# Kernel optimization log

Hardware: AMD Instinct MI355X
Metric: run time of the kernel (lower is better)

The kernel has to match this reference:

```python
import jax, jax.numpy as jnp
import numpy as np

DIMS = 3; B = 256; N = 256; K = 16; HID = 64; INC = 64; F = 64; EPG = 8192; DEPTH = 3
EPS = 1e-15


def setup_inputs() -> dict:
    key = jax.random.key(0)
    ks = jax.random.split(key, 16)
    E = B * EPG
    g = jnp.repeat(jnp.arange(B), EPG)
    row = (g * N + jax.random.randint(ks[0], (E,), 0, N)).astype(jnp.int32)
    col = (g * N + jax.random.randint(ks[1], (E,), 0, N)).astype(jnp.int32)
    edge_index = jnp.stack([row, col])
    edge_attr = jax.random.uniform(ks[2], (E, DIMS), dtype=jnp.float32)
    x = jax.random.normal(ks[3], (B * N, INC), dtype=jnp.float32)
    x_to_pool = jax.random.normal(ks[4], (B * N, F * DIMS), dtype=jnp.float32)
    batch = jnp.repeat(jnp.arange(B), N).astype(jnp.int32)
    def w(k, shape, fan):
        return (jax.random.normal(k, shape, dtype=jnp.float32) / np.float32(np.sqrt(fan)))
    return dict(
        x=x, edge_attr=edge_attr, x_to_pool=x_to_pool,
        Wm0=w(ks[5], (DIMS, INC, HID), INC), Ws0=w(ks[6], (DIMS, INC, HID), INC), b0=jnp.zeros((DIMS, HID), jnp.float32),
        Wm1=w(ks[7], (DIMS, HID, HID), HID), Ws1=w(ks[8], (DIMS, HID, HID), HID), b1=jnp.zeros((DIMS, HID), jnp.float32),
        Wm2=w(ks[9], (DIMS, HID, K), HID), Ws2=w(ks[10], (DIMS, HID, K), HID), b2=jnp.zeros((DIMS, K), jnp.float32),
        fcW1=w(ks[11], (HID * (DEPTH - 1) + K, 50), HID * (DEPTH - 1) + K), fcb1=jnp.zeros((50,), jnp.float32),
        fcW2=w(ks[12], (50, K), 50), fcb2=jnp.zeros((K,), jnp.float32),
        edge_index=edge_index, batch=batch,
    )


def reference(x, edge_attr, x_to_pool, Wm0, Ws0, b0, Wm1, Ws1, b1, Wm2, Ws2, b2,
              fcW1, fcb1, fcW2, fcb2, edge_index, batch):
    row, col = edge_index[0], edge_index[1]
    n_total = B * N

    # ---- batch_to_adj: scatter edge list into dense (dims, B, N, N) adjacency ----
    ge, rl, cl = row // N, row % N, col % N
    adj = jnp.zeros((DIMS, B, N, N), x.dtype).at[:, ge, rl, cl].add(edge_attr.T)

    # ---- ParallelResGraphConv: per-dim edge-weighted graph conv stack ----
    def gconv(h, we, Wm, Ws, b):
        agg = jax.ops.segment_sum(we[:, None] * h[col], row, num_segments=n_total)
        return jax.nn.relu(agg @ Wm + h @ Ws + b)

    assignments = []
    for d in range(DIMS):  # small fixed loop over parallel streams
        we = edge_attr[:, d]
        h0 = gconv(x, we, Wm0[d], Ws0[d], b0[d])
        h1 = gconv(h0, we, Wm1[d], Ws1[d], b1[d])
        h2 = gconv(h1, we, Wm2[d], Ws2[d], b2[d])
        conv_out = jnp.concatenate([h0, h1, h2], axis=-1)  # [BN, HID*2+K]
        logits = (conv_out @ fcW1 + fcb1) @ fcW2 + fcb2     # shared pool_fc
        assignments.append(logits)
    s = jax.nn.softmax(jnp.stack(assignments).reshape(DIMS, B, N, K), axis=-1)

    # ---- losses: modularity (edge gather) + entropy ----
    a_flat = s.reshape(DIMS, n_total, K)
    mod = jnp.float32(0.0)
    for d in range(DIMS):
        diff = a_flat[d, row] - a_flat[d, col]
        mod = mod + jnp.mean(edge_attr[:, d] * jnp.sum(diff * diff, axis=-1))
    ent = jnp.mean(jnp.sum(-s * jnp.log(s + EPS), axis=-1))
    loss = mod + ent

    # ---- DiffPool-style pooling ----
    xr = x_to_pool.reshape(n_total, F, DIMS)
    xr = jnp.transpose(xr, (2, 0, 1)).reshape(DIMS, B, N, F)
    px = jnp.einsum('dbnk,dbnf->dbkf', s, xr)
    tmp = jnp.einsum('dbnk,dbnm->dbkm', s, adj)
    padj = jnp.einsum('dbkm,dbml->dbkl', tmp, s)
    scale = jnp.float32(K / N)
    px = jnp.transpose(px, (1, 2, 3, 0)).reshape(B * K, F, DIMS) * scale
    padj = padj * (scale * scale)

    # ---- adj_to_tg_batch: dense pooled adjacency back to edge list (fixed shapes) ----
    rows = jnp.repeat(jnp.arange(K), K)
    cols = jnp.tile(jnp.arange(K), K)
    off = (jnp.arange(B) * K)[:, None]
    pei = jnp.stack([(off + rows[None, :]).reshape(-1), (off + cols[None, :]).reshape(-1)]).astype(jnp.int32)
    pea = jax.lax.stop_gradient(jnp.transpose(padj, (1, 2, 3, 0)).reshape(-1, DIMS))  # detach_pool=True
    pbatch = jnp.repeat(jnp.arange(B), K).astype(jnp.int32)
    return (px, pei, pea, pbatch, loss, s)
```

## Files before the change

### kernel.cpp

```cpp
#include <hip/hip_runtime.h>

#define DIMS 3
#define NB 256
#define NN 256
#define KK 16
#define HID 64
#define EPG 8192
#define NTOT (NB*NN)
#define NE (NB*EPG)

#define PX_OFF   0
#define PEI_OFF  786432
#define PEA_OFF  917504
#define PB_OFF   1114112
#define LOSS_OFF 1118208
#define S_OFF    1118209

#define WREC_WS  0
#define CLREC_WS 25165824
#define IPTR_WS  27262976
#define ENT_WS   27526144
#define MOD_WS   27529216
#define WC_WS    27532288
#define BC_WS    27541504

__global__ void fc_combine(const float* __restrict__ fcW1, const float* __restrict__ fcb1,
                           const float* __restrict__ fcW2, const float* __restrict__ fcb2,
                           float* __restrict__ wc, float* __restrict__ bc)
{
    const int t = threadIdx.x;
    for (int idx = t; idx < 144 * 16; idx += 256) {
        const int i = idx >> 4, k = idx & 15;
        float s = 0.f;
        for (int q = 0; q < 50; ++q) s += fcW1[i * 50 + q] * fcW2[q * 16 + k];
        wc[idx] = s;
    }
    if (t < 16) {
        float s = fcb2[t];
        for (int q = 0; q < 50; ++q) s += fcb1[q] * fcW2[q * 16 + t];
        bc[t] = s;
    }
}

#define HSTR 132
#define PSTR 129
__launch_bounds__(256)
__global__ void csr_build(const int* __restrict__ edge_index,
                          const float* __restrict__ edge_attr,
                          float* __restrict__ wrec, unsigned char* __restrict__ clrec,
                          int* __restrict__ indptr)
{
    __shared__ unsigned char  h[256 * HSTR];
    __shared__ unsigned short po[256 * PSTR];
    __shared__ int sc[256];
    const int b = blockIdx.x;
    const int t = threadIdx.x;
    const int* rowp = edge_index + (size_t)b * EPG;
    const int* colp = edge_index + (size_t)NB * EPG + (size_t)b * EPG;

    for (int i = t; i < 256 * HSTR / 4; i += 256) ((unsigned int*)h)[i] = 0u;
    __syncthreads();

    if (t < 128) {
        #pragma unroll 4
        for (int j = 0; j < 64; ++j) {
            const int r = rowp[t + 128 * j] & (NN - 1);
            h[r * HSTR + t]++;
        }
    }
    __syncthreads();

    int tot;
    {
        int s = 0;
        const unsigned int* hr = (const unsigned int*)(h + t * HSTR);
        #pragma unroll
        for (int c4 = 0; c4 < HSTR / 4; ++c4) {
            const unsigned int v = hr[c4];
            s += (v & 255) + ((v >> 8) & 255) + ((v >> 16) & 255) + (v >> 24);
        }
        tot = s;
        sc[t] = s;
    }
    __syncthreads();
    for (int ofs = 1; ofs < 256; ofs <<= 1) {
        int v = (t >= ofs) ? sc[t - ofs] : 0;
        __syncthreads();
        sc[t] += v;
        __syncthreads();
    }
    const int start = sc[t] - tot;
    indptr[b * 257 + t] = start;
    if (t == 255) indptr[b * 257 + 256] = EPG;

    {
        int run = start;
        #pragma unroll 4
        for (int c = 0; c < 128; ++c) {
            po[t * PSTR + c] = (unsigned short)run;
            run += h[t * HSTR + c];
        }
    }
    __syncthreads();

    if (t < 128) {
        const float* eap = edge_attr + (size_t)b * EPG * 3;
        float* w0 = wrec + (size_t)b * EPG;
        float* w1 = wrec + (size_t)NB * EPG + (size_t)b * EPG;
        float* w2 = wrec + 2 * (size_t)NB * EPG + (size_t)b * EPG;
        unsigned char* cdst = clrec + (size_t)b * EPG;
        #pragma unroll 2
        for (int j = 0; j < 64; ++j) {
            const int e = t + 128 * j;
            const int r = rowp[e] & (NN - 1);
            const int cl = colp[e] & (NN - 1);
            const int dest = po[r * PSTR + t]++;
            w0[dest] = eap[e * 3 + 0];
            w1[dest] = eap[e * 3 + 1];
            w2[dest] = eap[e * 3 + 2];
            cdst[dest] = (unsigned char)cl;
        }
    }
}

template<int OUTW, bool IS_L2>
__device__ __forceinline__ void layer_step(
    int t, int rp, int o, int js0, int je0, int je1,
    const float* __restrict__ wp, const unsigned char* __restrict__ clp,
    const float* __restrict__ Wm, const float* __restrict__ Ws,
    const float* __restrict__ bias, const float* __restrict__ wc,
    float4* hb4, float4* ab4, float* lgl)
{
    constexpr int NCO = OUTW / 8;
    const int r0 = rp * 2, r1 = r0 + 1;
    const int b0 = r0 * 16, s0 = r0 & 15;
    const int b1 = r1 * 16, s1 = r1 & 15;
    const int c0 = o * 2, c1 = o * 2 + 1;

    float ga0[8], ga1[8];
    #pragma unroll
    for (int u = 0; u < 8; ++u) { ga0[u] = 0.f; ga1[u] = 0.f; }
    for (int j = js0; j < je0; ++j) {
        const int cl = clp[j];
        const float w = wp[j];
        const int cb = cl * 16, cs = cl & 15;
        const float4 ha = hb4[cb + (c0 ^ cs)];
        const float4 hb = hb4[cb + (c1 ^ cs)];
        ga0[0] += w * ha.x; ga0[1] += w * ha.y; ga0[2] += w * ha.z; ga0[3] += w * ha.w;
        ga0[4] += w * hb.x; ga0[5] += w * hb.y; ga0[6] += w * hb.z; ga0[7] += w * hb.w;
    }
    for (int j = je0; j < je1; ++j) {
        const int cl = clp[j];
        const float w = wp[j];
        const int cb = cl * 16, cs = cl & 15;
        const float4 ha = hb4[cb + (c0 ^ cs)];
        const float4 hb = hb4[cb + (c1 ^ cs)];
        ga1[0] += w * ha.x; ga1[1] += w * ha.y; ga1[2] += w * ha.z; ga1[3] += w * ha.w;
        ga1[4] += w * hb.x; ga1[5] += w * hb.y; ga1[6] += w * hb.z; ga1[7] += w * hb.w;
    }
    {
        float4 v;
        v.x = ga0[0]; v.y = ga0[1]; v.z = ga0[2]; v.w = ga0[3]; ab4[b0 + (c0 ^ s0)] = v;
        v.x = ga0[4]; v.y = ga0[5]; v.z = ga0[6]; v.w = ga0[7]; ab4[b0 + (c1 ^ s0)] = v;
        v.x = ga1[0]; v.y = ga1[1]; v.z = ga1[2]; v.w = ga1[3]; ab4[b1 + (c0 ^ s1)] = v;
        v.x = ga1[4]; v.y = ga1[5]; v.z = ga1[6]; v.w = ga1[7]; ab4[b1 + (c1 ^ s1)] = v;
    }
    __syncthreads();

    const int j0 = o * NCO;
    float acc0[NCO], acc1[NCO];
    if constexpr (NCO == 8) {
        const float4 bv0 = *(const float4*)(bias + j0);
        const float4 bv1 = *(const float4*)(bias + j0 + 4);
        acc0[0]=bv0.x; acc0[1]=bv0.y; acc0[2]=bv0.z; acc0[3]=bv0.w;
        acc0[4]=bv1.x; acc0[5]=bv1.y; acc0[6]=bv1.z; acc0[7]=bv1.w;
        #pragma unroll
        for (int u = 0; u < 8; ++u) acc1[u] = acc0[u];
    } else {
        acc0[0] = bias[j0]; acc0[1] = bias[j0 + 1];
        acc1[0] = acc0[0];  acc1[1] = acc0[1];
    }
    #pragma unroll 1
    for (int ic = 0; ic < 16; ++ic) {
        const float4 h40 = hb4[b0 + (ic ^ s0)];
        const float4 h41 = hb4[b1 + (ic ^ s1)];
        const float hv0[4] = {h40.x, h40.y, h40.z, h40.w};
        const float hv1[4] = {h41.x, h41.y, h41.z, h41.w};
        #pragma unroll
        for (int u = 0; u < 4; ++u) {
            const float* wr = Ws + (ic * 4 + u) * OUTW + j0;
            const float a0 = hv0[u], a1 = hv1[u];
            if constexpr (NCO == 8) {
                const float4 wa = *(const float4*)(wr);
                const float4 wb = *(const float4*)(wr + 4);
                acc0[0]+=a0*wa.x; acc0[1]+=a0*wa.y; acc0[2]+=a0*wa.z; acc0[3]+=a0*wa.w;
                acc0[4]+=a0*wb.x; acc0[5]+=a0*wb.y; acc0[6]+=a0*wb.z; acc0[7]+=a0*wb.w;
                acc1[0]+=a1*wa.x; acc1[1]+=a1*wa.y; acc1[2]+=a1*wa.z; acc1[3]+=a1*wa.w;
                acc1[4]+=a1*wb.x; acc1[5]+=a1*wb.y; acc1[6]+=a1*wb.z; acc1[7]+=a1*wb.w;
            } else {
                const float2 w2 = *(const float2*)(wr);
                acc0[0]+=a0*w2.x; acc0[1]+=a0*w2.y;
                acc1[0]+=a1*w2.x; acc1[1]+=a1*w2.y;
            }
        }
    }
    #pragma unroll 1
    for (int ic = 0; ic < 16; ++ic) {
        const float4 a40 = ab4[b0 + (ic ^ s0)];
        const float4 a41 = ab4[b1 + (ic ^ s1)];
        const float av0[4] = {a40.x, a40.y, a40.z, a40.w};
        const float av1[4] = {a41.x, a41.y, a41.z, a41.w};
        #pragma unroll
        for (int u = 0; u < 4; ++u) {
            const float* wr = Wm + (ic * 4 + u) * OUTW + j0;
            const float a0 = av0[u], a1 = av1[u];
            if constexpr (NCO == 8) {
                const float4 wa = *(const float4*)(wr);
                const float4 wb = *(const float4*)(wr + 4);
                acc0[0]+=a0*wa.x; acc0[1]+=a0*wa.y; acc0[2]+=a0*wa.z; acc0[3]+=a0*wa.w;
                acc0[4]+=a0*wb.x; acc0[5]+=a0*wb.y; acc0[6]+=a0*wb.z; acc0[7]+=a0*wb.w;
                acc1[0]+=a1*wa.x; acc1[1]+=a1*wa.y; acc1[2]+=a1*wa.z; acc1[3]+=a1*wa.w;
                acc1[4]+=a1*wb.x; acc1[5]+=a1*wb.y; acc1[6]+=a1*wb.z; acc1[7]+=a1*wb.w;
            } else {
                const float2 w2 = *(const float2*)(wr);
                acc0[0]+=a0*w2.x; acc0[1]+=a0*w2.y;
                acc1[0]+=a1*w2.x; acc1[1]+=a1*w2.y;
            }
        }
    }
    #pragma unroll
    for (int jj = 0; jj < NCO; ++jj) {
        acc0[jj] = fmaxf(acc0[jj], 0.f);
        acc1[jj] = fmaxf(acc1[jj], 0.f);
    }
    __syncthreads();

    if constexpr (!IS_L2) {
        float4 v;
        v.x = acc0[0]; v.y = acc0[1]; v.z = acc0[2]; v.w = acc0[3]; hb4[b0 + (c0 ^ s0)] = v;
        v.x = acc0[4]; v.y = acc0[5]; v.z = acc0[6]; v.w = acc0[7]; hb4[b0 + (c1 ^ s0)] = v;
        v.x = acc1[0]; v.y = acc1[1]; v.z = acc1[2]; v.w = acc1[3]; hb4[b1 + (c0 ^ s1)] = v;
        v.x = acc1[4]; v.y = acc1[5]; v.z = acc1[6]; v.w = acc1[7]; hb4[b1 + (c1 ^ s1)] = v;
    } else {
        float* abf = (float*)ab4;
        const int cc = o >> 1, off = (o & 1) * 2;
        float* p0 = abf + (b0 + (cc ^ s0)) * 4 + off;
        float* p1 = abf + (b1 + (cc ^ s1)) * 4 + off;
        p0[0] = acc0[0]; p0[1] = acc0[1];
        p1[0] = acc1[0]; p1[1] = acc1[1];
    }
    __syncthreads();

    {
        const int r = t >> 2, kq = t & 3;
        const int rb = r * 16, rs = r & 15;
        float p[4] = {0.f, 0.f, 0.f, 0.f};
        if constexpr (!IS_L2) {
            #pragma unroll 2
            for (int c4 = 0; c4 < 16; ++c4) {
                const float4 v4 = hb4[rb + (c4 ^ rs)];
                const float vv[4] = {v4.x, v4.y, v4.z, v4.w};
                #pragma unroll
                for (int e = 0; e < 4; ++e) {
                    const float4 w4 = *(const float4*)(wc + (c4 * 4 + e) * 16 + kq * 4);
                    p[0] += vv[e] * w4.x; p[1] += vv[e] * w4.y;
                    p[2] += vv[e] * w4.z; p[3] += vv[e] * w4.w;
                }
            }
        } else {
            #pragma unroll 2
            for (int c4 = 0; c4 < 4; ++c4) {
                const float4 v4 = ab4[rb + (c4 ^ rs)];
                const float vv[4] = {v4.x, v4.y, v4.z, v4.w};
                #pragma unroll
                for (int e = 0; e < 4; ++e) {
                    const float4 w4 = *(const float4*)(wc + (c4 * 4 + e) * 16 + kq * 4);
                    p[0] += vv[e] * w4.x; p[1] += vv[e] * w4.y;
                    p[2] += vv[e] * w4.z; p[3] += vv[e] * w4.w;
                }
            }
        }
        float4* l4 = (float4*)lgl + r * 4 + kq;
        float4 old = *l4;
        old.x += p[0]; old.y += p[1]; old.z += p[2]; old.w += p[3];
        *l4 = old;
    }
}

__launch_bounds__(1024)
__global__ void gconv_kernel(
    const float* __restrict__ x,
    const float* __restrict__ Wm0, const float* __restrict__ Ws0, const float* __restrict__ b0,
    const float* __restrict__ Wm1, const float* __restrict__ Ws1, const float* __restrict__ b1,
    const float* __restrict__ Wm2, const float* __restrict__ Ws2, const float* __restrict__ b2,
    const float* __restrict__ wcomb, const float* __restrict__ bcomb,
    const float* __restrict__ wrec, const unsigned char* __restrict__ clrec,
    const int* __restrict__ indptr,
    float* __restrict__ out, float* __restrict__ entpart)
{
    __shared__ float4 hb4[4096];
    __shared__ float4 ab4[4096];
    __shared__ float  lgl[NN * 16];
    __shared__ float  red[16];
    const int t = threadIdx.x;
    const int bid = blockIdx.x;
    const int d = bid >> 8;
    const int b = bid & (NB - 1);
    const int rp = t >> 3;
    const int o = t & 7;
    const int lane = t & 63;
    const int wave = t >> 6;

    {
        const float4* xv = (const float4*)(x + (size_t)b * NN * HID);
        #pragma unroll
        for (int it = 0; it < 4; ++it) {
            const int idx = t + it * 1024;
            const int nrow = idx >> 4, c = idx & 15;
            hb4[nrow * 16 + (c ^ (nrow & 15))] = xv[idx];
        }
        #pragma unroll
        for (int it = 0; it < 4; ++it) lgl[t + it * 1024] = 0.f;
    }
    __syncthreads();

    const float* wp = wrec + (size_t)d * NB * EPG + (size_t)b * EPG;
    const unsigned char* clp = clrec + (size_t)b * EPG;
    const int js0 = indptr[b * 257 + rp * 2];
    const int je0 = indptr[b * 257 + rp * 2 + 1];
    const int je1 = indptr[b * 257 + rp * 2 + 2];

    layer_step<64, false>(t, rp, o, js0, je0, je1, wp, clp, Wm0 + d*HID*HID, Ws0 + d*HID*HID,
                          b0 + d*HID, wcomb,            hb4, ab4, lgl);
    layer_step<64, false>(t, rp, o, js0, je0, je1, wp, clp, Wm1 + d*HID*HID, Ws1 + d*HID*HID,
                          b1 + d*HID, wcomb + 64*16,    hb4, ab4, lgl);
    layer_step<16, true >(t, rp, o, js0, je0, je1, wp, clp, Wm2 + d*HID*KK,  Ws2 + d*HID*KK,
                          b2 + d*KK,  wcomb + 128*16,   hb4, ab4, lgl);
    __syncthreads();

    float ent_local = 0.f;
    if (t < 256) {
        const int rr = t;
        float logits[KK];
        const float* Lr = lgl + rr * 16;
        #pragma unroll
        for (int k = 0; k < KK; ++k) logits[k] = Lr[k] + bcomb[k];
        float m = logits[0];
        #pragma unroll
        for (int k = 1; k < KK; ++k) m = fmaxf(m, logits[k]);
        float sum = 0.f, sv[KK];
        #pragma unroll
        for (int k = 0; k < KK; ++k) { sv[k] = expf(logits[k] - m); sum += sv[k]; }
        const float inv = 1.f / sum;
        float4* sp4 = (float4*)(out + S_OFF + ((size_t)(d * NB + b) * NN + rr) * KK);
        #pragma unroll
        for (int q4 = 0; q4 < 4; ++q4) {
            float4 v;
            const float s0 = sv[q4*4+0] * inv, s1 = sv[q4*4+1] * inv;
            const float s2 = sv[q4*4+2] * inv, s3 = sv[q4*4+3] * inv;
            v.x = s0; v.y = s1; v.z = s2; v.w = s3;
            sp4[q4] = v;
            ent_local -= s0 * logf(s0 + 1e-15f) + s1 * logf(s1 + 1e-15f)
                       + s2 * logf(s2 + 1e-15f) + s3 * logf(s3 + 1e-15f);
        }
    }
    #pragma unroll
    for (int off = 32; off; off >>= 1) ent_local += __shfl_down(ent_local, off);
    if (lane == 0) red[wave] = ent_local;
    __syncthreads();
    if (t == 0) {
        float s = 0.f;
        #pragma unroll
        for (int w = 0; w < 16; ++w) s += red[w];
        entpart[bid] = s;
    }
}

#define SSTR 20
__launch_bounds__(256)
__global__ void pool_kernel(
    const float* __restrict__ x_to_pool,
    const float* __restrict__ wrec, const unsigned char* __restrict__ clrec,
    const int* __restrict__ indptr,
    const float* __restrict__ out_s, float* __restrict__ out, float* __restrict__ modpart)
{
    __shared__ float sl[NN * SSTR];
    __shared__ float gl[NN * SSTR];
    __shared__ float padjw[4 * 256];
    __shared__ float red[4];
    const int t = threadIdx.x;
    const int bid = blockIdx.x;
    const int d = bid >> 8;
    const int b = bid & (NB - 1);
    const int lane = t & 63;
    const int wave = t >> 6;

    {
        const float4* sp4 = (const float4*)(out_s + S_OFF + (size_t)(d * NB + b) * NN * KK);
        #pragma unroll
        for (int it = 0; it < 4; ++it) {
            const int idx = t + it * 256;
            const int nrow = idx >> 2, c = idx & 3;
            *(float4*)(sl + nrow * SSTR + c * 4) = sp4[idx];
        }
    }
    __syncthreads();

    const float* wp = wrec + (size_t)d * NB * EPG + (size_t)b * EPG;
    const unsigned char* clp = clrec + (size_t)b * EPG;
    const int js = indptr[b * 257 + t];
    const int je = indptr[b * 257 + t + 1];
    float sr[16];
    {
        #pragma unroll
        for (int c = 0; c < 4; ++c) {
            const float4 v = *(const float4*)(sl + t * SSTR + c * 4);
            sr[c*4+0] = v.x; sr[c*4+1] = v.y; sr[c*4+2] = v.z; sr[c*4+3] = v.w;
        }
    }
    float g[16];
    #pragma unroll
    for (int k = 0; k < 16; ++k) g[k] = 0.f;
    float modacc = 0.f;
    for (int j = js; j < je; ++j) {
        const int cl = clp[j];
        const float w = wp[j];
        const float* srow = sl + cl * SSTR;
        float ss = 0.f;
        #pragma unroll
        for (int c = 0; c < 4; ++c) {
            const float4 sv = *(const float4*)(srow + c * 4);
            g[c*4+0] += w * sv.x; g[c*4+1] += w * sv.y;
            g[c*4+2] += w * sv.z; g[c*4+3] += w * sv.w;
            const float d0 = sr[c*4+0] - sv.x, d1 = sr[c*4+1] - sv.y;
            const float d2 = sr[c*4+2] - sv.z, d3 = sr[c*4+3] - sv.w;
            ss += d0*d0 + d1*d1 + d2*d2 + d3*d3;
        }
        modacc += w * ss;
    }
    {
        #pragma unroll
        for (int c = 0; c < 4; ++c) {
            float4 v; v.x = g[c*4+0]; v.y = g[c*4+1]; v.z = g[c*4+2]; v.w = g[c*4+3];
            *(float4*)(gl + t * SSTR + c * 4) = v;
        }
    }
    __syncthreads();

    {
        const int k = t & 15, lg = (t >> 4) & 3;
        float p0 = 0.f, p1 = 0.f, p2 = 0.f, p3 = 0.f;
        const int r0 = wave * 64;
        for (int rr = r0; rr < r0 + 64; ++rr) {
            const float sk = sl[rr * SSTR + k];
            const float4 g4 = *(const float4*)(gl + rr * SSTR + lg * 4);
            p0 += sk * g4.x; p1 += sk * g4.y; p2 += sk * g4.z; p3 += sk * g4.w;
        }
        float* pw = padjw + wave * 256 + k * 16 + lg * 4;
        pw[0] = p0; pw[1] = p1; pw[2] = p2; pw[3] = p3;
    }

    {
        const int f = t & 63;
        const int kg = t >> 6;
        float xa0 = 0.f, xa1 = 0.f, xa2 = 0.f, xa3 = 0.f;
        const float* xp = x_to_pool + (size_t)b * NN * (64 * DIMS) + f * DIMS + d;
        #pragma unroll 4
        for (int nn2 = 0; nn2 < NN; ++nn2) {
            const float xv = xp[(size_t)nn2 * (64 * DIMS)];
            const float4 s4 = *(const float4*)(sl + nn2 * SSTR + kg * 4);
            xa0 += xv * s4.x; xa1 += xv * s4.y; xa2 += xv * s4.z; xa3 += xv * s4.w;
        }
        const float sc = 1.f / 16.f;
        out[PX_OFF + ((size_t)((b * KK + kg * 4 + 0) * 64) + f) * DIMS + d] = xa0 * sc;
        out[PX_OFF + ((size_t)((b * KK + kg * 4 + 1) * 64) + f) * DIMS + d] = xa1 * sc;
        out[PX_OFF + ((size_t)((b * KK + kg * 4 + 2) * 64) + f) * DIMS + d] = xa2 * sc;
        out[PX_OFF + ((size_t)((b * KK + kg * 4 + 3) * 64) + f) * DIMS + d] = xa3 * sc;
    }

    #pragma unroll
    for (int off = 32; off; off >>= 1) modacc += __shfl_down(modacc, off);
    if (lane == 0) red[wave] = modacc;
    __syncthreads();
    if (t == 0) modpart[bid] = red[0] + red[1] + red[2] + red[3];

    {
        const float v = (padjw[t] + padjw[256 + t] + padjw[512 + t] + padjw[768 + t]) * (1.f / 256.f);
        out[PEA_OFF + (size_t)((b * KK + (t >> 4)) * KK + (t & 15)) * DIMS + d] = v;
    }
}

__global__ void aux_kernel(float* __restrict__ out)
{
    const int idx = blockIdx.x * 256 + threadIdx.x;
    if (idx < 2 * NTOT) {
        const int r = idx & (NTOT - 1);
        const int bb = r >> 8;
        const int j = r & 255;
        const int v = (idx < NTOT) ? (bb * KK + (j >> 4)) : (bb * KK + (j & 15));
        out[PEI_OFF + idx] = (float)v;
    } else if (idx < 2 * NTOT + NB * KK) {
        const int i = idx - 2 * NTOT;
        out[PB_OFF + i] = (float)(i >> 4);
    }
}

__global__ void loss_kernel(const float* __restrict__ entpart,
                            const float* __restrict__ modpart,
                            float* __restrict__ out)
{
    const int tid = threadIdx.x;
    float e = 0.f, m = 0.f;
    for (int i = tid; i < DIMS * NB; i += 256) { e += entpart[i]; m += modpart[i]; }
    #pragma unroll
    for (int off = 32; off; off >>= 1) { e += __shfl_down(e, off); m += __shfl_down(m, off); }
    __shared__ float er[4], mr[4];
    const int wave = tid >> 6, lane = tid & 63;
    if (lane == 0) { er[wave] = e; mr[wave] = m; }
    __syncthreads();
    if (tid == 0) {
        const float es = er[0] + er[1] + er[2] + er[3];
        const float ms = mr[0] + mr[1] + mr[2] + mr[3];
        out[LOSS_OFF] = ms / (float)NE + es / (float)(DIMS * NTOT);
    }
}

extern "C" void kernel_launch(void* const* d_in, const int* in_sizes, int n_in,
                              void* d_out, int out_size, void* d_ws, size_t ws_size,
                              hipStream_t stream)
{
    const float* x         = (const float*)d_in[0];
    const float* edge_attr = (const float*)d_in[1];
    const float* x_to_pool = (const float*)d_in[2];
    const float* Wm0 = (const float*)d_in[3];
    const float* Ws0 = (const float*)d_in[4];
    const float* b0  = (const float*)d_in[5];
    const float* Wm1 = (const float*)d_in[6];
    const float* Ws1 = (const float*)d_in[7];
    const float* b1  = (const float*)d_in[8];
    const float* Wm2 = (const float*)d_in[9];
    const float* Ws2 = (const float*)d_in[10];
    const float* b2  = (const float*)d_in[11];
    const float* fcW1= (const float*)d_in[12];
    const float* fcb1= (const float*)d_in[13];
    const float* fcW2= (const float*)d_in[14];
    const float* fcb2= (const float*)d_in[15];
    const int* edge_index = (const int*)d_in[16];
    float* out = (float*)d_out;
    char* ws = (char*)d_ws;
    float*         wrec  = (float*)(ws + WREC_WS);
    unsigned char* clrec = (unsigned char*)(ws + CLREC_WS);
    int*           iptr  = (int*)(ws + IPTR_WS);
    float*         entpart = (float*)(ws + ENT_WS);
    float*         modpart = (float*)(ws + MOD_WS);
    float*         wc    = (float*)(ws + WC_WS);
    float*         bc    = (float*)(ws + BC_WS);

    csr_build<<<dim3(NB), dim3(256), 0, stream>>>(edge_index, edge_attr, wrec, clrec, iptr);
    fc_combine<<<dim3(1), dim3(256), 0, stream>>>(fcW1, fcb1, fcW2, fcb2, wc, bc);
    gconv_kernel<<<dim3(DIMS * NB), dim3(1024), 0, stream>>>(
        x, Wm0, Ws0, b0, Wm1, Ws1, b1, Wm2, Ws2, b2,
        wc, bc, wrec, clrec, iptr, out, entpart);
    pool_kernel<<<dim3(DIMS * NB), dim3(256), 0, stream>>>(
        x_to_pool, wrec, clrec, iptr, out, out, modpart);
    aux_kernel<<<dim3((2 * NTOT + NB * KK + 255) / 256), dim3(256), 0, stream>>>(out);
    loss_kernel<<<dim3(1), dim3(256), 0, stream>>>(entpart, modpart, out);
}
```

Baseline: 596.3 us.

## Alias aggregation buffer onto hidden buffer and keep logits in registers

Drops the separate ab4 aggregation buffer and the lgl logits buffer from shared memory. The Ws·h product is now computed first, then the aggregated neighbour features overwrite the hidden buffer in place, and the per-layer logit contributions accumulate in registers, written to shared memory once at the end with a padded stride. This cuts shared memory per block from about 144KB to about 64KB, which could let two 1024-thread blocks share a CU. It adds an extra barrier per layer.

New measurement: 581.2 us. 2.5% less time.

```diff
diff --git a/kernel.cpp b/kernel.cpp
--- a/kernel.cpp
+++ b/kernel.cpp
@@ -125,11 +125,11 @@
 
 template<int OUTW, bool IS_L2>
 __device__ __forceinline__ void layer_step(
-    int t, int rp, int o, int js0, int je0, int je1,
+    int rp, int o, int fr, int fkq, int js0, int je0, int je1,
     const float* __restrict__ wp, const unsigned char* __restrict__ clp,
     const float* __restrict__ Wm, const float* __restrict__ Ws,
     const float* __restrict__ bias, const float* __restrict__ wc,
-    float4* hb4, float4* ab4, float* lgl)
+    float4* hb4, float* p)
 {
     constexpr int NCO = OUTW / 8;
     const int r0 = rp * 2, r1 = r0 + 1;
@@ -158,14 +158,6 @@
         ga1[0] += w * ha.x; ga1[1] += w * ha.y; ga1[2] += w * ha.z; ga1[3] += w * ha.w;
         ga1[4] += w * hb.x; ga1[5] += w * hb.y; ga1[6] += w * hb.z; ga1[7] += w * hb.w;
     }
-    {
-        float4 v;
-        v.x = ga0[0]; v.y = ga0[1]; v.z = ga0[2]; v.w = ga0[3]; ab4[b0 + (c0 ^ s0)] = v;
-        v.x = ga0[4]; v.y = ga0[5]; v.z = ga0[6]; v.w = ga0[7]; ab4[b0 + (c1 ^ s0)] = v;
-        v.x = ga1[0]; v.y = ga1[1]; v.z = ga1[2]; v.w = ga1[3]; ab4[b1 + (c0 ^ s1)] = v;
-        v.x = ga1[4]; v.y = ga1[5]; v.z = ga1[6]; v.w = ga1[7]; ab4[b1 + (c1 ^ s1)] = v;
-    }
-    __syncthreads();
 
     const int j0 = o * NCO;
     float acc0[NCO], acc1[NCO];
@@ -204,10 +196,21 @@
             }
         }
     }
+    __syncthreads();
+
+    {
+        float4 v;
+        v.x = ga0[0]; v.y = ga0[1]; v.z = ga0[2]; v.w = ga0[3]; hb4[b0 + (c0 ^ s0)] = v;
+        v.x = ga0[4]; v.y = ga0[5]; v.z = ga0[6]; v.w = ga0[7]; hb4[b0 + (c1 ^ s0)] = v;
+        v.x = ga1[0]; v.y = ga1[1]; v.z = ga1[2]; v.w = ga1[3]; hb4[b1 + (c0 ^ s1)] = v;
+        v.x = ga1[4]; v.y = ga1[5]; v.z = ga1[6]; v.w = ga1[7]; hb4[b1 + (c1 ^ s1)] = v;
+    }
+    __syncthreads();
+
     #pragma unroll 1
     for (int ic = 0; ic < 16; ++ic) {
-        const float4 a40 = ab4[b0 + (ic ^ s0)];
-        const float4 a41 = ab4[b1 + (ic ^ s1)];
+        const float4 a40 = hb4[b0 + (ic ^ s0)];
+        const float4 a41 = hb4[b1 + (ic ^ s1)];
         const float av0[4] = {a40.x, a40.y, a40.z, a40.w};
         const float av1[4] = {a41.x, a41.y, a41.z, a41.w};
         #pragma unroll
@@ -242,19 +245,17 @@
         v.x = acc1[0]; v.y = acc1[1]; v.z = acc1[2]; v.w = acc1[3]; hb4[b1 + (c0 ^ s1)] = v;
         v.x = acc1[4]; v.y = acc1[5]; v.z = acc1[6]; v.w = acc1[7]; hb4[b1 + (c1 ^ s1)] = v;
     } else {
-        float* abf = (float*)ab4;
+        float* hbf = (float*)hb4;
         const int cc = o >> 1, off = (o & 1) * 2;
-        float* p0 = abf + (b0 + (cc ^ s0)) * 4 + off;
-        float* p1 = abf + (b1 + (cc ^ s1)) * 4 + off;
+        float* p0 = hbf + (b0 + (cc ^ s0)) * 4 + off;
+        float* p1 = hbf + (b1 + (cc ^ s1)) * 4 + off;
         p0[0] = acc0[0]; p0[1] = acc0[1];
         p1[0] = acc1[0]; p1[1] = acc1[1];
     }
     __syncthreads();
 
     {
-        const int r = t >> 2, kq = t & 3;
-        const int rb = r * 16, rs = r & 15;
-        float p[4] = {0.f, 0.f, 0.f, 0.f};
+        const int rb = fr * 16, rs = fr & 15;
         if constexpr (!IS_L2) {
             #pragma unroll 2
             for (int c4 = 0; c4 < 16; ++c4) {
@@ -262,7 +263,7 @@
                 const float vv[4] = {v4.x, v4.y, v4.z, v4.w};
                 #pragma unroll
                 for (int e = 0; e < 4; ++e) {
-                    const float4 w4 = *(const float4*)(wc + (c4 * 4 + e) * 16 + kq * 4);
+                    const float4 w4 = *(const float4*)(wc + (c4 * 4 + e) * 16 + fkq * 4);
                     p[0] += vv[e] * w4.x; p[1] += vv[e] * w4.y;
                     p[2] += vv[e] * w4.z; p[3] += vv[e] * w4.w;
                 }
@@ -270,20 +271,16 @@
         } else {
             #pragma unroll 2
             for (int c4 = 0; c4 < 4; ++c4) {
-                const float4 v4 = ab4[rb + (c4 ^ rs)];
+                const float4 v4 = hb4[rb + (c4 ^ rs)];
                 const float vv[4] = {v4.x, v4.y, v4.z, v4.w};
                 #pragma unroll
                 for (int e = 0; e < 4; ++e) {
-                    const float4 w4 = *(const float4*)(wc + (c4 * 4 + e) * 16 + kq * 4);
+                    const float4 w4 = *(const float4*)(wc + (c4 * 4 + e) * 16 + fkq * 4);
                     p[0] += vv[e] * w4.x; p[1] += vv[e] * w4.y;
                     p[2] += vv[e] * w4.z; p[3] += vv[e] * w4.w;
                 }
             }
         }
-        float4* l4 = (float4*)lgl + r * 4 + kq;
-        float4 old = *l4;
-        old.x += p[0]; old.y += p[1]; old.z += p[2]; old.w += p[3];
-        *l4 = old;
     }
 }
 
@@ -299,8 +296,6 @@
     float* __restrict__ out, float* __restrict__ entpart)
 {
     __shared__ float4 hb4[4096];
-    __shared__ float4 ab4[4096];
-    __shared__ float  lgl[NN * 16];
     __shared__ float  red[16];
     const int t = threadIdx.x;
     const int bid = blockIdx.x;
@@ -308,6 +303,8 @@
     const int b = bid & (NB - 1);
     const int rp = t >> 3;
     const int o = t & 7;
+    const int fr = t >> 2;
+    const int fkq = t & 3;
     const int lane = t & 63;
     const int wave = t >> 6;
 
@@ -319,9 +316,8 @@
             const int nrow = idx >> 4, c = idx & 15;
             hb4[nrow * 16 + (c ^ (nrow & 15))] = xv[idx];
         }
-        #pragma unroll
-        for (int it = 0; it < 4; ++it) lgl[t + it * 1024] = 0.f;
-    }
+    }
+    float p[4] = {0.f, 0.f, 0.f, 0.f};
     __syncthreads();
 
     const float* wp = wrec + (size_t)d * NB * EPG + (size_t)b * EPG;
@@ -330,19 +326,26 @@
     const int je0 = indptr[b * 257 + rp * 2 + 1];
     const int je1 = indptr[b * 257 + rp * 2 + 2];
 
-    layer_step<64, false>(t, rp, o, js0, je0, je1, wp, clp, Wm0 + d*HID*HID, Ws0 + d*HID*HID,
-                          b0 + d*HID, wcomb,            hb4, ab4, lgl);
-    layer_step<64, false>(t, rp, o, js0, je0, je1, wp, clp, Wm1 + d*HID*HID, Ws1 + d*HID*HID,
-                          b1 + d*HID, wcomb + 64*16,    hb4, ab4, lgl);
-    layer_step<16, true >(t, rp, o, js0, je0, je1, wp, clp, Wm2 + d*HID*KK,  Ws2 + d*HID*KK,
-                          b2 + d*KK,  wcomb + 128*16,   hb4, ab4, lgl);
+    layer_step<64, false>(rp, o, fr, fkq, js0, je0, je1, wp, clp, Wm0 + d*HID*HID,
+                          Ws0 + d*HID*HID, b0 + d*HID, wcomb,          hb4, p);
+    layer_step<64, false>(rp, o, fr, fkq, js0, je0, je1, wp, clp, Wm1 + d*HID*HID,
+                          Ws1 + d*HID*HID, b1 + d*HID, wcomb + 64*16,  hb4, p);
+    layer_step<16, true >(rp, o, fr, fkq, js0, je0, je1, wp, clp, Wm2 + d*HID*KK,
+                          Ws2 + d*HID*KK,  b2 + d*KK,  wcomb + 128*16, hb4, p);
+
+    __syncthreads();
+    {
+        float* hbf = (float*)hb4;
+        float* dst = hbf + fr * 17 + fkq * 4;
+        dst[0] = p[0]; dst[1] = p[1]; dst[2] = p[2]; dst[3] = p[3];
+    }
     __syncthreads();
 
     float ent_local = 0.f;
     if (t < 256) {
         const int rr = t;
+        const float* Lr = (const float*)hb4 + rr * 17;
         float logits[KK];
-        const float* Lr = lgl + rr * 16;
         #pragma unroll
         for (int k = 0; k < KK; ++k) logits[k] = Lr[k] + bcomb[k];
         float m = logits[0];
```
